# Optimization experiments

Measured on AMD Instinct MI355X. Metric: run time of the kernel, lower is better.

## Reference

```python
import jax, jax.numpy as jnp
import numpy as np

D_MODEL = 1024
NHEAD = 16
HEAD_DIM = D_MODEL // NHEAD
MLP_DIM = 4096
ROPE_THETA = 10000.0


def layer_norm(x, g, b, eps=1e-5):
    mu = jnp.mean(x, axis=-1, keepdims=True)
    var = jnp.var(x, axis=-1, keepdims=True)
    return (x - mu) * jax.lax.rsqrt(var + eps) * g + b


def rope_cos_sin(seq_len, dim):
    # lucidrains RotaryEmbedding: inv_freq over even indices, freqs repeated interleaved
    inv_freq = 1.0 / (ROPE_THETA ** (jnp.arange(0, dim, 2, dtype=jnp.float32) / dim))
    t = jnp.arange(seq_len, dtype=jnp.float32)
    freqs = t[:, None] * inv_freq[None, :]            # (S, dim/2)
    freqs = jnp.repeat(freqs, 2, axis=-1)             # (S, dim) interleaved [f0,f0,f1,f1,...]
    return jnp.cos(freqs), jnp.sin(freqs)


def apply_rope(x, cos, sin):
    # x: (B, S, H, D); interleaved rotate_half: (x0,x1) -> (-x1, x0)
    x1 = x[..., ::2]
    x2 = x[..., 1::2]
    rot = jnp.stack([-x2, x1], axis=-1).reshape(x.shape)
    c = cos[None, :, None, :]
    s = sin[None, :, None, :]
    return x * c + rot * s


def setup_inputs() -> dict:
    key = jax.random.key(0)
    ks = jax.random.split(key, 8)
    B, S = 2, 2048
    sc = 1.0 / np.sqrt(D_MODEL)
    inputs = jax.random.normal(ks[0], (B, S, D_MODEL), dtype=jnp.float32)
    return {
        "inputs": inputs,
        "ln1_g": jnp.ones((D_MODEL,), jnp.float32),
        "ln1_b": jnp.zeros((D_MODEL,), jnp.float32),
        "Wq": jax.random.normal(ks[1], (D_MODEL, D_MODEL), jnp.float32) * sc,
        "Wk": jax.random.normal(ks[2], (D_MODEL, D_MODEL), jnp.float32) * sc,
        "Wv": jax.random.normal(ks[3], (D_MODEL, D_MODEL), jnp.float32) * sc,
        "Wo": jax.random.normal(ks[4], (D_MODEL, D_MODEL), jnp.float32) * sc,
        "ln2_g": jnp.ones((D_MODEL,), jnp.float32),
        "ln2_b": jnp.zeros((D_MODEL,), jnp.float32),
        "Wfc2": jax.random.normal(ks[5], (D_MODEL, MLP_DIM), jnp.float32) * sc,
        "bfc2": jnp.zeros((MLP_DIM,), jnp.float32),
        "Wfc3": jax.random.normal(ks[6], (MLP_DIM, D_MODEL), jnp.float32) * (1.0 / np.sqrt(MLP_DIM)),
        "bfc3": jnp.zeros((D_MODEL,), jnp.float32),
    }


def reference(inputs, ln1_g, ln1_b, Wq, Wk, Wv, Wo, ln2_g, ln2_b, Wfc2, bfc2, Wfc3, bfc3):
    B, S, _ = inputs.shape
    x = layer_norm(inputs, ln1_g, ln1_b)
    q = (x @ Wq).reshape(B, S, NHEAD, HEAD_DIM)
    k = (x @ Wk).reshape(B, S, NHEAD, HEAD_DIM)
    v = (x @ Wv).reshape(B, S, NHEAD, HEAD_DIM)
    cos, sin = rope_cos_sin(S, HEAD_DIM)
    q = apply_rope(q, cos, sin)
    k = apply_rope(k, cos, sin)
    scores = jnp.einsum('bqhd,bkhd->bhqk', q, k) / np.sqrt(HEAD_DIM)
    attn = jax.nn.softmax(scores, axis=-1)
    out = jnp.einsum('bhqk,bkhd->bqhd', attn, v).reshape(B, S, D_MODEL)
    out = out @ Wo
    mlp_in = out + inputs
    h = layer_norm(mlp_in, ln2_g, ln2_b)
    h = jax.nn.gelu(h @ Wfc2 + bfc2, approximate=False)
    h = h @ Wfc3 + bfc3
    return h + mlp_in
```

## Files before the change

### kernel.cpp

```cpp
#include <hip/hip_runtime.h>
#include <cstdint>
#include <cstddef>

typedef __bf16 bf16x8 __attribute__((ext_vector_type(8)));
typedef __bf16 bf16x4 __attribute__((ext_vector_type(4)));
typedef float  f32x4  __attribute__((ext_vector_type(4)));
typedef float  f32x16 __attribute__((ext_vector_type(16)));
typedef unsigned int u32x4 __attribute__((ext_vector_type(4)));

__device__ __forceinline__ void load16_to_lds(const void* g, void* l) {
  __builtin_amdgcn_global_load_lds(
      (const __attribute__((address_space(1))) void*)g,
      (__attribute__((address_space(3))) void*)l, 16, 0, 0);
}

__device__ __forceinline__ unsigned cvt_pk_bf16(float a, float b) {
  unsigned r;
  asm("v_cvt_pk_bf16_f32 %0, %1, %2" : "=v"(r) : "v"(a), "v"(b));
  return r;
}
__device__ __forceinline__ void permlane32_swap(unsigned &a, unsigned &b) {
  asm("v_permlane32_swap_b32 %0, %1" : "+v"(a), "+v"(b));
}

__global__ __launch_bounds__(256) void transpose_cast(
    const float* __restrict__ src, __bf16* __restrict__ dst, int K, int N)
{
  __shared__ float tile[32][33];
  const int n0 = blockIdx.x * 32, k0 = blockIdx.y * 32;
  const int tx = threadIdx.x, ty = threadIdx.y;
#pragma unroll
  for (int i = 0; i < 32; i += 8)
    tile[ty + i][tx] = src[(size_t)(k0 + ty + i) * N + n0 + tx];
  __syncthreads();
#pragma unroll
  for (int i = 0; i < 32; i += 8)
    dst[(size_t)(n0 + ty + i) * K + k0 + tx] = (__bf16)tile[tx][ty + i];
}

__global__ __launch_bounds__(256) void transpose_cast_qkv(
    const float* __restrict__ s0, const float* __restrict__ s1,
    const float* __restrict__ s2, __bf16* __restrict__ dst)
{
  __shared__ float tile[32][33];
  const float* src = blockIdx.z == 0 ? s0 : blockIdx.z == 1 ? s1 : s2;
  __bf16* d = dst + (size_t)blockIdx.z * 1024 * 1024;
  const int n0 = blockIdx.x * 32, k0 = blockIdx.y * 32;
  const int tx = threadIdx.x, ty = threadIdx.y;
#pragma unroll
  for (int i = 0; i < 32; i += 8)
    tile[ty + i][tx] = src[(size_t)(k0 + ty + i) * 1024 + n0 + tx];
  __syncthreads();
#pragma unroll
  for (int i = 0; i < 32; i += 8)
    d[(size_t)(n0 + ty + i) * 1024 + k0 + tx] = (__bf16)tile[tx][ty + i];
}

__global__ __launch_bounds__(256) void ln_kernel(
    const float* __restrict__ x, const float* __restrict__ g,
    const float* __restrict__ bta, __bf16* __restrict__ out)
{
  const int row = blockIdx.x;
  const int t = threadIdx.x;
  const float4 v = ((const float4*)(x + (size_t)row * 1024))[t];
  float s  = v.x + v.y + v.z + v.w;
  float ss = v.x * v.x + v.y * v.y + v.z * v.z + v.w * v.w;
#pragma unroll
  for (int o = 32; o > 0; o >>= 1) { s += __shfl_down(s, o); ss += __shfl_down(ss, o); }
  __shared__ float rs[4], rss[4];
  const int w = t >> 6, l = t & 63;
  if (l == 0) { rs[w] = s; rss[w] = ss; }
  __syncthreads();
  s  = rs[0] + rs[1] + rs[2] + rs[3];
  ss = rss[0] + rss[1] + rss[2] + rss[3];
  const float mu = s * (1.0f / 1024.0f);
  const float var = ss * (1.0f / 1024.0f) - mu * mu;
  const float rstd = rsqrtf(var + 1e-5f);
  const float4 gg = ((const float4*)g)[t];
  const float4 bb = ((const float4*)bta)[t];
  __bf16* o = out + (size_t)row * 1024 + t * 4;
  o[0] = (__bf16)((v.x - mu) * rstd * gg.x + bb.x);
  o[1] = (__bf16)((v.y - mu) * rstd * gg.y + bb.y);
  o[2] = (__bf16)((v.z - mu) * rstd * gg.z + bb.z);
  o[3] = (__bf16)((v.w - mu) * rstd * gg.w + bb.w);
}

enum { EPI_BF16 = 0, EPI_RES_F32 = 1, EPI_GELU_BF16 = 2, EPI_BIAS_RES_F32 = 3 };

template <int TM, int KB, int EPI>
__global__ __launch_bounds__(256, 2) void gemm_bf16(
    const __bf16* __restrict__ A, const __bf16* __restrict__ Bt,
    __bf16* __restrict__ outb, float* __restrict__ outf,
    const float* __restrict__ bias, const float* __restrict__ res,
    int M, int N, int K)
{
  constexpr int MT = TM / 32;
  constexpr int KS = KB / 32;
  __shared__ __bf16 As0[TM * KB], As1[TM * KB];
  __shared__ __bf16 Bs0[128 * KB], Bs1[128 * KB];
  const int tid  = threadIdx.x;
  const int lane = tid & 63, w = tid >> 6;
  const int wm = w >> 1, wn = w & 1;
  const int quad = lane >> 4, l16 = lane & 15;
  const int m0 = blockIdx.y * TM, n0 = blockIdx.x * 128;

  f32x4 acc[MT][4] = {};
  const __bf16* Ag = A  + (size_t)m0 * K;
  const __bf16* Bg = Bt + (size_t)n0 * K;

#define G_STAGE(AsX, BsX, k0) {                                            \
    _Pragma("unroll")                                                      \
    for (int r2 = 0; r2 < TM * KB / 2048; ++r2) {                          \
      const int c = r2 * 256 + tid;                                        \
      const int r = c / (KB / 8), cb = c % (KB / 8);                       \
      const int g = (KB == 64) ? (cb ^ (r & 7)) : cb;                      \
      load16_to_lds(Ag + (size_t)r * K + (k0) + g * 8, &AsX[c * 8]);       \
    }                                                                      \
    _Pragma("unroll")                                                      \
    for (int r2 = 0; r2 < KB / 16; ++r2) {                                 \
      const int c = r2 * 256 + tid;                                        \
      const int r = c / (KB / 8), cb = c % (KB / 8);                       \
      const int g = (KB == 64) ? (cb ^ (r & 7)) : cb;                      \
      load16_to_lds(Bg + (size_t)r * K + (k0) + g * 8, &BsX[c * 8]);       \
    } }

#define G_COMPUTE(AsX, BsX) {                                              \
    bf16x8 af[MT][KS], bfr[4][KS];                                         \
    _Pragma("unroll")                                                      \
    for (int mt = 0; mt < MT; ++mt) {                                      \
      const int row = wm * (TM / 2) + mt * 16 + l16;                       \
      _Pragma("unroll")                                                    \
      for (int ks = 0; ks < KS; ++ks) {                                    \
        const int ch = (KB == 64) ? ((ks * 4 + quad) ^ (row & 7)) : quad;  \
        af[mt][ks] = *(const bf16x8*)&AsX[row * KB + ch * 8];              \
      }                                                                    \
    }                                                                      \
    _Pragma("unroll")                                                      \
    for (int nt = 0; nt < 4; ++nt) {                                       \
      const int row = wn * 64 + nt * 16 + l16;                             \
      _Pragma("unroll")                                                    \
      for (int ks = 0; ks < KS; ++ks) {                                    \
        const int ch = (KB == 64) ? ((ks * 4 + quad) ^ (row & 7)) : quad;  \
        bfr[nt][ks] = *(const bf16x8*)&BsX[row * KB + ch * 8];             \
      }                                                                    \
    }                                                                      \
    _Pragma("unroll")                                                      \
    for (int ks = 0; ks < KS; ++ks)                                        \
      _Pragma("unroll")                                                    \
      for (int mt = 0; mt < MT; ++mt)                                      \
        _Pragma("unroll")                                                  \
        for (int nt = 0; nt < 4; ++nt)                                     \
          acc[mt][nt] = __builtin_amdgcn_mfma_f32_16x16x32_bf16(           \
              af[mt][ks], bfr[nt][ks], acc[mt][nt], 0, 0, 0);              \
  }

  G_STAGE(As0, Bs0, 0);
  const int nk = K / KB;
  for (int kt = 0; kt < nk; kt += 2) {
    __syncthreads();
    if (kt + 1 < nk) G_STAGE(As1, Bs1, (kt + 1) * KB);
    G_COMPUTE(As0, Bs0);
    __syncthreads();
    if (kt + 2 < nk) G_STAGE(As0, Bs0, (kt + 2) * KB);
    G_COMPUTE(As1, Bs1);
  }
#undef G_STAGE
#undef G_COMPUTE

#pragma unroll
  for (int mt = 0; mt < MT; ++mt) {
#pragma unroll
    for (int nt = 0; nt < 4; ++nt) {
      const int col = n0 + wn * 64 + nt * 16 + l16;
#pragma unroll
      for (int i = 0; i < 4; ++i) {
        const int row = m0 + wm * (TM / 2) + mt * 16 + quad * 4 + i;
        float v = acc[mt][nt][i];
        const size_t idx = (size_t)row * N + col;
        if (EPI == EPI_BF16) {
          outb[idx] = (__bf16)v;
        } else if (EPI == EPI_RES_F32) {
          outf[idx] = v + res[idx];
        } else if (EPI == EPI_GELU_BF16) {
          v += bias[col];
          outb[idx] = (__bf16)(0.5f * v * (1.0f + erff(v * 0.70710678118f)));
        } else {
          v += bias[col];
          outf[idx] = v + res[idx];
        }
      }
    }
  }
}

template <int EPI>
__global__ __launch_bounds__(512, 1) void gemm_bf16_256p(
    const __bf16* __restrict__ A, const __bf16* __restrict__ Bt,
    __bf16* __restrict__ outb, const float* __restrict__ bias,
    int M, int N, int K)
{
  __shared__ __bf16 As0[256 * 32], As1[256 * 32], As2[256 * 32], As3[256 * 32];
  __shared__ __bf16 Bs0[256 * 32], Bs1[256 * 32], Bs2[256 * 32], Bs3[256 * 32];
  const int tid  = threadIdx.x;
  const int lane = tid & 63, w = tid >> 6;
  const int wm = w >> 2, wn = w & 3;
  const int quad = lane >> 4, l16 = lane & 15;
  const int m0 = blockIdx.y * 256, n0 = blockIdx.x * 256;

  f32x4 acc[8][4] = {};
  const __bf16* Ag = A  + (size_t)m0 * K;
  const __bf16* Bg = Bt + (size_t)n0 * K;

#define P_STAGE(AsX, BsX, t) {                                             \
    const int k0 = (t) * 32;                                               \
    _Pragma("unroll")                                                      \
    for (int r2 = 0; r2 < 2; ++r2) {                                       \
      const int c = r2 * 512 + tid;                                        \
      const int r = c >> 2, cb = c & 3;                                    \
      load16_to_lds(Ag + (size_t)r * K + k0 + cb * 8, &AsX[c * 8]);        \
    }                                                                      \
    _Pragma("unroll")                                                      \
    for (int r2 = 0; r2 < 2; ++r2) {                                       \
      const int c = r2 * 512 + tid;                                        \
      const int r = c >> 2, cb = c & 3;                                    \
      load16_to_lds(Bg + (size_t)r * K + k0 + cb * 8, &BsX[c * 8]);        \
    } }

#define P_COMPUTE(AsX, BsX) {                                              \
    bf16x8 af[8], bfr[4];                                                  \
    _Pragma("unroll")                                                      \
    for (int mt = 0; mt < 8; ++mt)                                         \
      af[mt] = *(const bf16x8*)&AsX[(wm * 128 + mt * 16 + l16) * 32 + quad * 8]; \
    _Pragma("unroll")                                                      \
    for (int nt = 0; nt < 4; ++nt)                                         \
      bfr[nt] = *(const bf16x8*)&BsX[(wn * 64 + nt * 16 + l16) * 32 + quad * 8]; \
    __builtin_amdgcn_s_setprio(1);                                         \
    _Pragma("unroll")                                                      \
    for (int mt = 0; mt < 8; ++mt)                                         \
      _Pragma("unroll")                                                    \
      for (int nt = 0; nt < 4; ++nt)                                       \
        acc[mt][nt] = __builtin_amdgcn_mfma_f32_16x16x32_bf16(             \
            af[mt], bfr[nt], acc[mt][nt], 0, 0, 0);                        \
    __builtin_amdgcn_s_setprio(0);                                         \
  }

#define P_WAITBAR(NTOK) {                                                  \
    asm volatile("s_waitcnt vmcnt(" NTOK ")" ::: "memory");                \
    __builtin_amdgcn_s_barrier();                                          \
    asm volatile("" ::: "memory");                                         \
  }

  P_STAGE(As0, Bs0, 0);
  P_STAGE(As1, Bs1, 1);
  P_STAGE(As2, Bs2, 2);
  const int nk = K / 32;
  int kt = 0;
  for (; kt + 8 <= nk; kt += 4) {
    P_WAITBAR("8");  P_STAGE(As3, Bs3, kt + 3);  P_COMPUTE(As0, Bs0);
    P_WAITBAR("8");  P_STAGE(As0, Bs0, kt + 4);  P_COMPUTE(As1, Bs1);
    P_WAITBAR("8");  P_STAGE(As1, Bs1, kt + 5);  P_COMPUTE(As2, Bs2);
    P_WAITBAR("8");  P_STAGE(As2, Bs2, kt + 6);  P_COMPUTE(As3, Bs3);
  }
  P_WAITBAR("8");  P_STAGE(As3, Bs3, kt + 3);  P_COMPUTE(As0, Bs0);
  P_WAITBAR("8");  P_COMPUTE(As1, Bs1);
  P_WAITBAR("4");  P_COMPUTE(As2, Bs2);
  P_WAITBAR("0");  P_COMPUTE(As3, Bs3);
#undef P_STAGE
#undef P_COMPUTE
#undef P_WAITBAR

#pragma unroll
  for (int mt = 0; mt < 8; ++mt) {
#pragma unroll
    for (int nt = 0; nt < 4; ++nt) {
      const int col = n0 + wn * 64 + nt * 16 + l16;
#pragma unroll
      for (int i = 0; i < 4; ++i) {
        const int row = m0 + wm * 128 + mt * 16 + quad * 4 + i;
        float v = acc[mt][nt][i];
        const size_t idx = (size_t)row * N + col;
        if (EPI == EPI_BF16) {
          outb[idx] = (__bf16)v;
        } else if (EPI == EPI_GELU_BF16) {
          v += bias[col];
          outb[idx] = (__bf16)(0.5f * v * (1.0f + erff(v * 0.70710678118f)));
        }
      }
    }
  }
}

__global__ __launch_bounds__(256) void rope_qk(
    const __bf16* __restrict__ qkv, __bf16* __restrict__ qr, __bf16* __restrict__ kr)
{
  const int idx = blockIdx.x * 256 + threadIdx.x;
  const int d2 = idx & 31;
  const int h  = (idx >> 5) & 15;
  const int bs = idx >> 9;
  const int s  = bs & 2047;
  const int b  = bs >> 11;
  const float inv_freq = exp2f(-((float)d2 * (1.0f / 32.0f)) * 13.2877123795f);
  const float ang = (float)s * inv_freq;
  const float c = cosf(ang), sn = sinf(ang);
  const float QS = 0.125f * 1.44269504f;
  const __bf16* qp = qkv + (size_t)bs * 3072 + h * 64 + 2 * d2;
  const __bf16* kp = qp + 1024;
  const float q0 = (float)qp[0], q1 = (float)qp[1];
  const float k0 = (float)kp[0], k1 = (float)kp[1];
  const size_t o = ((size_t)(b * 16 + h) * 2048 + s) * 64 + 2 * d2;
  qr[o]     = (__bf16)((q0 * c - q1 * sn) * QS);
  qr[o + 1] = (__bf16)((q1 * c + q0 * sn) * QS);
  kr[o]     = (__bf16)(k0 * c - k1 * sn);
  kr[o + 1] = (__bf16)(k1 * c + k0 * sn);
}

__global__ __launch_bounds__(256) void v_transpose(
    const __bf16* __restrict__ qkv, __bf16* __restrict__ vt)
{
  __shared__ __bf16 t[64][66];
  const int st = blockIdx.x, h = blockIdx.y, b = blockIdx.z;
  const int tx = threadIdx.x & 63, ty = threadIdx.x >> 6;
  const int s0 = st * 64;
  const __bf16* src = qkv + ((size_t)(b * 2048 + s0)) * 3072 + 2048 + h * 64;
#pragma unroll
  for (int i = 0; i < 64; i += 4)
    t[ty + i][tx] = src[(size_t)(ty + i) * 3072 + tx];
  __syncthreads();
  __bf16* dst = vt + ((size_t)(b * 16 + h) * 64) * 2048 + s0;
#pragma unroll
  for (int i = 0; i < 64; i += 4)
    dst[(size_t)(ty + i) * 2048 + tx] = t[tx][ty + i];
}

__global__ __launch_bounds__(256, 2) void attn_kernel(
    const __bf16* __restrict__ qr, const __bf16* __restrict__ kr,
    const __bf16* __restrict__ vt, __bf16* __restrict__ attn_o)
{
  constexpr int S = 2048, DH = 64, NH = 16, BQ = 128, BKK = 64;
  __shared__ __align__(16) __bf16 Qs[BQ * 64];
  __shared__ __align__(16) __bf16 Ks0[64 * 64], Ks1[64 * 64], Ks2[64 * 64], Ks3[64 * 64];
  __shared__ __align__(16) __bf16 Vts0[64 * 64], Vts1[64 * 64], Vts2[64 * 64], Vts3[64 * 64];

  const int tid = threadIdx.x;
  const int lane = tid & 63, w = tid >> 6;
  const int l32 = lane & 31, half = lane >> 5;
  const int qt = blockIdx.x, h = blockIdx.y, b = blockIdx.z;
  const int bh = b * NH + h;
  const __bf16* Q  = qr + ((size_t)bh * S + qt * BQ) * DH;
  const __bf16* Kp = kr + (size_t)bh * S * DH;
  const __bf16* Vp = vt + (size_t)bh * DH * S;
  __bf16* Pb = Qs + w * 2048;

#define A_STAGE(KsX, VtsX, kk) {                                           \
    _Pragma("unroll")                                                      \
    for (int r2 = 0; r2 < 2; ++r2) {                                       \
      const int c = r2 * 256 + tid;                                        \
      const int r = c >> 3, cb = c & 7;                                    \
      const int cg = (cb ^ (r & 7)) * 8;                                   \
      load16_to_lds(Kp + (size_t)((kk) + r) * DH + cg, &KsX[c * 8]);       \
      load16_to_lds(Vp + (size_t)r * S + (kk) + cg, &VtsX[c * 8]);         \
    } }

#pragma unroll
  for (int r4 = 0; r4 < 4; ++r4) {
    const int c = r4 * 256 + tid;
    const int r = c >> 3, cb = c & 7;
    load16_to_lds(Q + (size_t)r * DH + ((cb ^ (r & 7)) * 8), &Qs[c * 8]);
  }
  A_STAGE(Ks0, Vts0, 0);
  A_STAGE(Ks1, Vts1, BKK);
  __syncthreads();

  bf16x8 qfB[4];
  {
    const int row = w * 32 + l32;
#pragma unroll
    for (int c = 0; c < 4; ++c)
      qfB[c] = *(const bf16x8*)&Qs[row * 64 + (((2 * c + half) ^ (row & 7)) * 8)];
  }

  float mreg = -3.0e38f, lreg = 0.0f;
  f32x16 oacc[2] = {};
  const f32x16 zz = {};
  f32x16 saA[2], saB[2];

#define A_QK(KsX, saX) {                                                   \
    bf16x8 kf[2][4];                                                       \
    _Pragma("unroll")                                                      \
    for (int t = 0; t < 2; ++t) {                                          \
      const int row = 32 * t + l32;                                        \
      _Pragma("unroll")                                                    \
      for (int c = 0; c < 4; ++c)                                          \
        kf[t][c] = *(const bf16x8*)&KsX[row * 64 + (((2 * c + half) ^ (l32 & 7)) * 8)]; \
    }                                                                      \
    __builtin_amdgcn_s_setprio(1);                                         \
    _Pragma("unroll")                                                      \
    for (int t = 0; t < 2; ++t) {                                          \
      saX[t] = __builtin_amdgcn_mfma_f32_32x32x16_bf16(kf[t][0], qfB[0], zz, 0, 0, 0); \
      _Pragma("unroll")                                                    \
      for (int c = 1; c < 4; ++c)                                          \
        saX[t] = __builtin_amdgcn_mfma_f32_32x32x16_bf16(kf[t][c], qfB[c], saX[t], 0, 0, 0); \
    }                                                                      \
    __builtin_amdgcn_s_setprio(0);                                         \
  }

#define A_SMPV(saC, VtsX) {                                                \
    bf16x8 vf[2][4];                                                       \
    _Pragma("unroll")                                                      \
    for (int v = 0; v < 2; ++v) {                                          \
      const int row = 32 * v + l32;                                        \
      _Pragma("unroll")                                                    \
      for (int c = 0; c < 4; ++c)                                          \
        vf[v][c] = *(const bf16x8*)&VtsX[row * 64 + (((2 * c + half) ^ (l32 & 7)) * 8)]; \
    }                                                                      \
    float pm[8];                                                           \
    _Pragma("unroll")                                                      \
    for (int t = 0; t < 2; ++t)                                            \
      _Pragma("unroll")                                                    \
      for (int g = 0; g < 4; ++g)                                          \
        pm[t * 4 + g] = fmaxf(fmaxf(saC[t][4 * g], saC[t][4 * g + 1]),     \
                              fmaxf(saC[t][4 * g + 2], saC[t][4 * g + 3]));\
    float mx = fmaxf(fmaxf(fmaxf(pm[0], pm[1]), fmaxf(pm[2], pm[3])),      \
                     fmaxf(fmaxf(pm[4], pm[5]), fmaxf(pm[6], pm[7])));     \
    mx = fmaxf(mx, __shfl_xor(mx, 32));                                    \
    float mnew = mreg;                                                     \
    if (!__all(mx <= mreg + 8.0f)) {                                       \
      mnew = fmaxf(mreg, mx);                                              \
      const float alpha = __builtin_amdgcn_exp2f(mreg - mnew);             \
      mreg = mnew;                                                         \
      lreg *= alpha;                                                       \
      _Pragma("unroll")                                                    \
      for (int v = 0; v < 2; ++v)                                          \
        _Pragma("unroll")                                                  \
        for (int r = 0; r < 16; ++r) oacc[v][r] *= alpha;                  \
    }                                                                      \
    float ps0 = 0.f, ps1 = 0.f, ps2 = 0.f, ps3 = 0.f;                      \
    _Pragma("unroll")                                                      \
    for (int t = 0; t < 2; ++t)                                            \
      _Pragma("unroll")                                                    \
      for (int r = 0; r < 16; r += 4) {                                    \
        const float p0 = __builtin_amdgcn_exp2f(saC[t][r]     - mnew);     \
        const float p1 = __builtin_amdgcn_exp2f(saC[t][r + 1] - mnew);     \
        const float p2 = __builtin_amdgcn_exp2f(saC[t][r + 2] - mnew);     \
        const float p3 = __builtin_amdgcn_exp2f(saC[t][r + 3] - mnew);     \
        saC[t][r] = p0; saC[t][r + 1] = p1;                                \
        saC[t][r + 2] = p2; saC[t][r + 3] = p3;                            \
        ps0 += p0; ps1 += p1; ps2 += p2; ps3 += p3;                        \
      }                                                                    \
    __builtin_amdgcn_s_setprio(1);                                         \
    _Pragma("unroll")                                                      \
    for (int c = 0; c < 4; ++c) {                                          \
      const int t = c >> 1, r0 = (c & 1) * 8;                              \
      unsigned px = cvt_pk_bf16(saC[t][r0],     saC[t][r0 + 1]);           \
      unsigned py = cvt_pk_bf16(saC[t][r0 + 2], saC[t][r0 + 3]);           \
      unsigned pz = cvt_pk_bf16(saC[t][r0 + 4], saC[t][r0 + 5]);           \
      unsigned pw = cvt_pk_bf16(saC[t][r0 + 6], saC[t][r0 + 7]);           \
      permlane32_swap(px, pz);                                             \
      permlane32_swap(py, pw);                                             \
      const u32x4 pv4 = { px, py, pz, pw };                                \
      const bf16x8 pf = __builtin_bit_cast(bf16x8, pv4);                   \
      oacc[0] = __builtin_amdgcn_mfma_f32_32x32x16_bf16(vf[0][c], pf, oacc[0], 0, 0, 0); \
      oacc[1] = __builtin_amdgcn_mfma_f32_32x32x16_bf16(vf[1][c], pf, oacc[1], 0, 0, 0); \
    }                                                                      \
    __builtin_amdgcn_s_setprio(0);                                         \
    float sum = (ps0 + ps1) + (ps2 + ps3);                                 \
    sum += __shfl_xor(sum, 32);                                            \
    lreg += sum;                                                           \
  }

#define A_PHASE(KsNext, VtsCur, KsSt, VtsSt, saCur, saNext, kkSt, DO_QK, DO_ST) { \
    __syncthreads();                                                       \
    if (DO_ST) A_STAGE(KsSt, VtsSt, kkSt);                                 \
    if (DO_QK) A_QK(KsNext, saNext);                                       \
    A_SMPV(saCur, VtsCur);                                                 \
  }

  A_QK(Ks0, saA);

  for (int p = 0; p < 28; p += 4) {
    A_PHASE(Ks1, Vts0, Ks2, Vts2, saA, saB, (p + 2) * BKK, true, true);
    A_PHASE(Ks2, Vts1, Ks3, Vts3, saB, saA, (p + 3) * BKK, true, true);
    A_PHASE(Ks3, Vts2, Ks0, Vts0, saA, saB, (p + 4) * BKK, true, true);
    A_PHASE(Ks0, Vts3, Ks1, Vts1, saB, saA, (p + 5) * BKK, true, true);
  }
  A_PHASE(Ks1, Vts0, Ks2, Vts2, saA, saB, 30 * BKK, true, true);
  A_PHASE(Ks2, Vts1, Ks3, Vts3, saB, saA, 31 * BKK, true, true);
  A_PHASE(Ks3, Vts2, Ks0, Vts0, saA, saB, 0,        true, false);
  A_PHASE(Ks0, Vts3, Ks1, Vts1, saB, saA, 0,        false, false);
#undef A_STAGE
#undef A_QK
#undef A_SMPV
#undef A_PHASE

  const float linv = 1.0f / lreg;
#pragma unroll
  for (int v = 0; v < 2; ++v)
#pragma unroll
    for (int g = 0; g < 4; ++g) {
      bf16x4 ov;
#pragma unroll
      for (int i = 0; i < 4; ++i) ov[i] = (__bf16)(oacc[v][4 * g + i] * linv);
      const int dc = 4 * v + g;
      *(bf16x4*)&Pb[l32 * 64 + ((dc ^ (l32 & 7)) * 8) + 4 * half] = ov;
    }
#pragma unroll
  for (int cc = 0; cc < 4; ++cc) {
    const int c = cc * 64 + lane;
    const int r = c >> 3, g = c & 7;
    const bf16x8 od = *(const bf16x8*)&Pb[r * 64 + ((g ^ (r & 7)) * 8)];
    const int srow = qt * BQ + w * 32 + r;
    *(bf16x8*)&attn_o[((size_t)b * S + srow) * 1024 + h * 64 + g * 8] = od;
  }
}

extern "C" void kernel_launch(void* const* d_in, const int* in_sizes, int n_in,
                              void* d_out, int out_size, void* d_ws, size_t ws_size,
                              hipStream_t stream) {
  const float* inputs = (const float*)d_in[0];
  const float* ln1_g  = (const float*)d_in[1];
  const float* ln1_b  = (const float*)d_in[2];
  const float* Wq     = (const float*)d_in[3];
  const float* Wk     = (const float*)d_in[4];
  const float* Wv     = (const float*)d_in[5];
  const float* Wo     = (const float*)d_in[6];
  const float* ln2_g  = (const float*)d_in[7];
  const float* ln2_b  = (const float*)d_in[8];
  const float* Wfc2   = (const float*)d_in[9];
  const float* bfc2   = (const float*)d_in[10];
  const float* Wfc3   = (const float*)d_in[11];
  const float* bfc3   = (const float*)d_in[12];
  float* out = (float*)d_out;
  char* ws = (char*)d_ws;
  const size_t MB = 1024 * 1024;

  __bf16* Wqkv_t = (__bf16*)(ws);
  __bf16* Wo_t   = (__bf16*)(ws + 6 * MB);
  __bf16* Wfc2_t = (__bf16*)(ws + 8 * MB);
  __bf16* Wfc3_t = (__bf16*)(ws + 16 * MB);
  __bf16* xb     = (__bf16*)(ws + 24 * MB);
  __bf16* attn_o = xb;
  __bf16* qkv    = (__bf16*)(ws + 32 * MB);
  float*  mlp_in = (float*)(ws + 32 * MB);
  __bf16* h2     = (__bf16*)(ws + 48 * MB);
  __bf16* qrb    = (__bf16*)(ws + 56 * MB);
  __bf16* krb    = (__bf16*)(ws + 64 * MB);
  __bf16* vtb    = (__bf16*)(ws + 72 * MB);
  __bf16* hbuf   = (__bf16*)(ws + 56 * MB);

  const dim3 tb(32, 8);
  transpose_cast_qkv<<<dim3(32, 32, 3), tb, 0, stream>>>(Wq, Wk, Wv, Wqkv_t);
  transpose_cast<<<dim3(32, 32),  tb, 0, stream>>>(Wo,   Wo_t,   1024, 1024);
  transpose_cast<<<dim3(128, 32), tb, 0, stream>>>(Wfc2, Wfc2_t, 1024, 4096);
  transpose_cast<<<dim3(32, 128), tb, 0, stream>>>(Wfc3, Wfc3_t, 4096, 1024);

  ln_kernel<<<4096, 256, 0, stream>>>(inputs, ln1_g, ln1_b, xb);

  gemm_bf16_256p<EPI_BF16><<<dim3(12, 16), 512, 0, stream>>>(
      xb, Wqkv_t, qkv, nullptr, 4096, 3072, 1024);

  rope_qk<<<8192, 256, 0, stream>>>(qkv, qrb, krb);
  v_transpose<<<dim3(32, 16, 2), 256, 0, stream>>>(qkv, vtb);

  attn_kernel<<<dim3(16, 16, 2), 256, 0, stream>>>(qrb, krb, vtb, attn_o);

  gemm_bf16<64, 64, EPI_RES_F32><<<dim3(8, 64), 256, 0, stream>>>(
      attn_o, Wo_t, nullptr, mlp_in, nullptr, inputs, 4096, 1024, 1024);

  ln_kernel<<<4096, 256, 0, stream>>>(mlp_in, ln2_g, ln2_b, h2);

  gemm_bf16_256p<EPI_GELU_BF16><<<dim3(16, 16), 512, 0, stream>>>(
      h2, Wfc2_t, hbuf, bfc2, 4096, 4096, 1024);

  gemm_bf16<64, 64, EPI_BIAS_RES_F32><<<dim3(8, 64), 256, 0, stream>>>(
      hbuf, Wfc3_t, nullptr, out, bfc3, mlp_in, 4096, 1024, 4096);
}
```

Measured before the change: 352.6 us.

## Restructure 256x256 GEMM into double-buffered BK=64 ping-pong with swizzled LDS

Replaces the 4-stage BK=32 pipeline of the 256x256 bf16 GEMM with a 2-buffer BK=64 scheme. Each k-tile's MFMA work is split into quadrants interleaved with global-to-LDS staging. LDS rows are XOR-swizzled to avoid bank conflicts, and fragments are read with explicit ds_read_b128. Explicit barriers and sched_barriers order loads against compute, at the cost of more barriers and a hardcoded K=1024 loop count (8 iterations of 2 tiles).

```diff
diff --git a/kernel.cpp b/kernel.cpp
--- a/kernel.cpp
+++ b/kernel.cpp
@@ -12,6 +12,15 @@
   __builtin_amdgcn_global_load_lds(
       (const __attribute__((address_space(1))) void*)g,
       (__attribute__((address_space(3))) void*)l, 16, 0, 0);
+}
+
+__device__ __forceinline__ bf16x8 lds_read_b128(unsigned addr) {
+  u32x4 r;
+  asm volatile("ds_read_b128 %0, %1" : "=v"(r) : "v"(addr));
+  return __builtin_bit_cast(bf16x8, r);
+}
+__device__ __forceinline__ unsigned lds_off(const void* p) {
+  return (unsigned)(size_t)(const __attribute__((address_space(3))) void*)p;
 }
 
 __device__ __forceinline__ unsigned cvt_pk_bf16(float a, float b) {
@@ -194,13 +203,13 @@
 }
 
 template <int EPI>
-__global__ __launch_bounds__(512, 1) void gemm_bf16_256p(
+__global__ __launch_bounds__(512, 1) void gemm_bf16_256p8(
     const __bf16* __restrict__ A, const __bf16* __restrict__ Bt,
     __bf16* __restrict__ outb, const float* __restrict__ bias,
     int M, int N, int K)
 {
-  __shared__ __bf16 As0[256 * 32], As1[256 * 32], As2[256 * 32], As3[256 * 32];
-  __shared__ __bf16 Bs0[256 * 32], Bs1[256 * 32], Bs2[256 * 32], Bs3[256 * 32];
+  __shared__ __align__(16) __bf16 Ad0[256 * 64], Ad1[256 * 64];
+  __shared__ __align__(16) __bf16 Bd0[256 * 64], Bd1[256 * 64];
   const int tid  = threadIdx.x;
   const int lane = tid & 63, w = tid >> 6;
   const int wm = w >> 2, wn = w & 3;
@@ -211,63 +220,119 @@
   const __bf16* Ag = A  + (size_t)m0 * K;
   const __bf16* Bg = Bt + (size_t)n0 * K;
 
-#define P_STAGE(AsX, BsX, t) {                                             \
-    const int k0 = (t) * 32;                                               \
+  const unsigned swz = (unsigned)((quad ^ (l16 & 7)) * 16);
+  const unsigned aB0 = lds_off(Ad0) + (wm * 128 + l16) * 128 + swz;
+  const unsigned aB1 = lds_off(Ad1) + (wm * 128 + l16) * 128 + swz;
+  const unsigned bB0 = lds_off(Bd0) + (wn * 64 + l16) * 128 + swz;
+  const unsigned bB1 = lds_off(Bd1) + (wn * 64 + l16) * 128 + swz;
+
+  bf16x8 af[4][2], bfr[4][2];
+
+#define STG_A(ARR, t, h) {                                                 \
     _Pragma("unroll")                                                      \
     for (int r2 = 0; r2 < 2; ++r2) {                                       \
       const int c = r2 * 512 + tid;                                        \
-      const int r = c >> 2, cb = c & 3;                                    \
-      load16_to_lds(Ag + (size_t)r * K + k0 + cb * 8, &AsX[c * 8]);        \
-    }                                                                      \
+      const int r = c >> 3, cb = c & 7;                                    \
+      const int g = cb ^ (r & 7);                                          \
+      load16_to_lds(Ag + (size_t)((h) * 128 + r) * K + (t) * 64 + g * 8,   \
+                    &ARR[(h) * 8192 + c * 8]);                             \
+    } }
+#define STG_B(ARR, t, h) {                                                 \
     _Pragma("unroll")                                                      \
     for (int r2 = 0; r2 < 2; ++r2) {                                       \
       const int c = r2 * 512 + tid;                                        \
-      const int r = c >> 2, cb = c & 3;                                    \
-      load16_to_lds(Bg + (size_t)r * K + k0 + cb * 8, &BsX[c * 8]);        \
+      const int r = c >> 3, cb = c & 7;                                    \
+      const int g = cb ^ (r & 7);                                          \
+      load16_to_lds(Bg + (size_t)((h) * 128 + r) * K + (t) * 64 + g * 8,   \
+                    &ARR[(h) * 8192 + c * 8]);                             \
     } }
 
-#define P_COMPUTE(AsX, BsX) {                                              \
-    bf16x8 af[8], bfr[4];                                                  \
-    _Pragma("unroll")                                                      \
-    for (int mt = 0; mt < 8; ++mt)                                         \
-      af[mt] = *(const bf16x8*)&AsX[(wm * 128 + mt * 16 + l16) * 32 + quad * 8]; \
-    _Pragma("unroll")                                                      \
-    for (int nt = 0; nt < 4; ++nt)                                         \
-      bfr[nt] = *(const bf16x8*)&BsX[(wn * 64 + nt * 16 + l16) * 32 + quad * 8]; \
+#define A_READ(base, hi) {                                                 \
+    _Pragma("unroll")                                                      \
+    for (int mt = 0; mt < 4; ++mt) {                                       \
+      const unsigned a0 = (base) + (hi) * 8192 + mt * 2048;                \
+      af[mt][0] = lds_read_b128(a0);                                       \
+      af[mt][1] = lds_read_b128(a0 ^ 64);                                  \
+    } }
+#define B_READ(base, nh) {                                                 \
+    _Pragma("unroll")                                                      \
+    for (int k2 = 0; k2 < 2; ++k2) {                                       \
+      const int nt = (nh) * 2 + k2;                                        \
+      const unsigned b0 = (base) + nt * 2048;                              \
+      bfr[nt][0] = lds_read_b128(b0);                                      \
+      bfr[nt][1] = lds_read_b128(b0 ^ 64);                                 \
+    } }
+
+#define MFMA_Q(mh, nh) {                                                   \
     __builtin_amdgcn_s_setprio(1);                                         \
     _Pragma("unroll")                                                      \
-    for (int mt = 0; mt < 8; ++mt)                                         \
-      _Pragma("unroll")                                                    \
-      for (int nt = 0; nt < 4; ++nt)                                       \
-        acc[mt][nt] = __builtin_amdgcn_mfma_f32_16x16x32_bf16(             \
-            af[mt], bfr[nt], acc[mt][nt], 0, 0, 0);                        \
+    for (int ks = 0; ks < 2; ++ks)                                         \
+      _Pragma("unroll")                                                    \
+      for (int mtl = 0; mtl < 4; ++mtl)                                    \
+        _Pragma("unroll")                                                  \
+        for (int ntl = 0; ntl < 2; ++ntl)                                  \
+          acc[(mh) * 4 + mtl][(nh) * 2 + ntl] =                            \
+              __builtin_amdgcn_mfma_f32_16x16x32_bf16(                     \
+                  af[mtl][ks], bfr[(nh) * 2 + ntl][ks],                    \
+                  acc[(mh) * 4 + mtl][(nh) * 2 + ntl], 0, 0, 0);           \
     __builtin_amdgcn_s_setprio(0);                                         \
   }
 
-#define P_WAITBAR(NTOK) {                                                  \
-    asm volatile("s_waitcnt vmcnt(" NTOK ")" ::: "memory");                \
-    __builtin_amdgcn_s_barrier();                                          \
-    asm volatile("" ::: "memory");                                         \
-  }
-
-  P_STAGE(As0, Bs0, 0);
-  P_STAGE(As1, Bs1, 1);
-  P_STAGE(As2, Bs2, 2);
-  const int nk = K / 32;
-  int kt = 0;
-  for (; kt + 8 <= nk; kt += 4) {
-    P_WAITBAR("8");  P_STAGE(As3, Bs3, kt + 3);  P_COMPUTE(As0, Bs0);
-    P_WAITBAR("8");  P_STAGE(As0, Bs0, kt + 4);  P_COMPUTE(As1, Bs1);
-    P_WAITBAR("8");  P_STAGE(As1, Bs1, kt + 5);  P_COMPUTE(As2, Bs2);
-    P_WAITBAR("8");  P_STAGE(As2, Bs2, kt + 6);  P_COMPUTE(As3, Bs3);
-  }
-  P_WAITBAR("8");  P_STAGE(As3, Bs3, kt + 3);  P_COMPUTE(As0, Bs0);
-  P_WAITBAR("8");  P_COMPUTE(As1, Bs1);
-  P_WAITBAR("4");  P_COMPUTE(As2, Bs2);
-  P_WAITBAR("0");  P_COMPUTE(As3, Bs3);
-#undef P_STAGE
-#undef P_COMPUTE
-#undef P_WAITBAR
+#define SBAR()  asm volatile("s_barrier" ::: "memory")
+#define LGKM0() { asm volatile("s_waitcnt lgkmcnt(0)" ::: "memory");       \
+                  __builtin_amdgcn_sched_barrier(0); }
+#define SCH0()  __builtin_amdgcn_sched_barrier(0)
+#define VMW(N)  asm volatile("s_waitcnt vmcnt(" N ")" ::: "memory")
+
+#define P8_BODY(LAST, t0) {                                                \
+                                                       \
+    A_READ(aB0, 0); B_READ(bB0, 0); STG_A(Ad1, (t0) + 1, 0);               \
+    SBAR(); LGKM0(); MFMA_Q(0, 0); SCH0(); SBAR();                         \
+                                                       \
+    B_READ(bB0, 1); STG_A(Ad1, (t0) + 1, 1);                               \
+    SBAR(); LGKM0(); MFMA_Q(0, 1); SCH0(); SBAR();                         \
+                                                       \
+    A_READ(aB0, 1); if (!(LAST)) STG_B(Bd0, (t0) + 2, 0);                  \
+    SBAR(); LGKM0(); MFMA_Q(1, 0); SCH0(); SBAR();                         \
+                                      \
+    if (!(LAST)) STG_B(Bd0, (t0) + 2, 1);                                  \
+    SBAR(); LGKM0(); MFMA_Q(1, 1); SCH0();                                 \
+    if (LAST) { VMW("0"); } else { VMW("4"); }                             \
+    SBAR();                                                                \
+                                                       \
+    A_READ(aB1, 0); B_READ(bB1, 0); if (!(LAST)) STG_A(Ad0, (t0) + 2, 0);  \
+    SBAR(); LGKM0(); MFMA_Q(0, 0); SCH0(); SBAR();                         \
+                                                       \
+    B_READ(bB1, 1); if (!(LAST)) STG_A(Ad0, (t0) + 2, 1);                  \
+    SBAR(); LGKM0(); MFMA_Q(0, 1); SCH0(); SBAR();                         \
+                                                       \
+    A_READ(aB1, 1); if (!(LAST)) STG_B(Bd1, (t0) + 3, 0);                  \
+    SBAR(); LGKM0(); MFMA_Q(1, 0); SCH0(); SBAR();                         \
+                                      \
+    if (!(LAST)) STG_B(Bd1, (t0) + 3, 1);                                  \
+    SBAR(); LGKM0(); MFMA_Q(1, 1); SCH0();                                 \
+    if (!(LAST)) { VMW("4"); }                                             \
+    SBAR();                                                                \
+  }
+
+  STG_B(Bd0, 0, 0); STG_B(Bd0, 0, 1);
+  STG_A(Ad0, 0, 0); STG_A(Ad0, 0, 1);
+  STG_B(Bd1, 1, 0); STG_B(Bd1, 1, 1);
+  VMW("4"); SBAR();
+
+  for (int j = 0; j < 7; ++j) { P8_BODY(false, 2 * j); }
+  P8_BODY(true, 14);
+
+#undef STG_A
+#undef STG_B
+#undef A_READ
+#undef B_READ
+#undef MFMA_Q
+#undef SBAR
+#undef LGKM0
+#undef SCH0
+#undef VMW
+#undef P8_BODY
 
 #pragma unroll
   for (int mt = 0; mt < 8; ++mt) {
@@ -555,7 +620,7 @@
 
   ln_kernel<<<4096, 256, 0, stream>>>(inputs, ln1_g, ln1_b, xb);
 
-  gemm_bf16_256p<EPI_BF16><<<dim3(12, 16), 512, 0, stream>>>(
+  gemm_bf16_256p8<EPI_BF16><<<dim3(12, 16), 512, 0, stream>>>(
       xb, Wqkv_t, qkv, nullptr, 4096, 3072, 1024);
 
   rope_qk<<<8192, 256, 0, stream>>>(qkv, qrb, krb);
@@ -568,7 +633,7 @@
 
   ln_kernel<<<4096, 256, 0, stream>>>(mlp_in, ln2_g, ln2_b, h2);
 
-  gemm_bf16_256p<EPI_GELU_BF16><<<dim3(16, 16), 512, 0, stream>>>(
+  gemm_bf16_256p8<EPI_GELU_BF16><<<dim3(16, 16), 512, 0, stream>>>(
       h2, Wfc2_t, hbuf, bfc2, 4096, 4096, 1024);
 
   gemm_bf16<64, 64, EPI_BIAS_RES_F32><<<dim3(8, 64), 256, 0, stream>>>(
```

After: 374.6 us. 1.06x slower.
